# Performance work log

Hardware: AMD Instinct MI355X
Metric: run time of the kernel (lower is better)

The kernel has to match this reference:

```python
import jax, jax.numpy as jnp
import numpy as np

B, S, E, H, V = 64, 400, 512, 512, 32000


def setup_inputs() -> dict:
    key = jax.random.key(0)
    ks = jax.random.split(key, 16)
    sc = lambda fan: 1.0 / np.sqrt(fan)
    u = lambda k, shape, fan: jax.random.uniform(k, shape, jnp.float32, -sc(fan), sc(fan))
    mask = jax.random.randint(ks[3], (B, S), 0, 2).astype(bool)
    mask = mask.at[:, 0].set(True)  # ensure at least one valid position per row
    return {
        "decoder_input": jax.random.normal(ks[0], (B, E), jnp.float32),
        "previous_hidden_state": jax.random.normal(ks[1], (B, H), jnp.float32),
        "encoder_output": jax.random.normal(ks[2], (B, S, 2 * H), jnp.float32),
        "mask": mask,
        # GRUCell params (torch layout: weight_ih [3H,E], weight_hh [3H,H])
        "w_ih": u(ks[4], (3 * H, E), H),
        "w_hh": u(ks[5], (3 * H, H), H),
        "b_ih": u(ks[6], (3 * H,), H),
        "b_hh": u(ks[7], (3 * H,), H),
        # Attention params
        "Wh_w": u(ks[8], (H, 2 * H), 2 * H),
        "Wh_b": u(ks[9], (H,), 2 * H),
        "Ws_w": u(ks[10], (H, H), H),
        "Ws_b": u(ks[11], (H,), H),
        "vatt_w": u(ks[12], (1, H), H),  # Linear(H,1,bias=False)
        # Output projections
        "V_w": u(ks[13], (H, 3 * H), 3 * H),
        "V_b": u(ks[13], (H,), 3 * H),
        "Vhat_w": u(ks[14], (V, H), H),
        "Vhat_b": u(ks[15], (V,), H),
    }


def reference(decoder_input, previous_hidden_state, encoder_output, mask,
              w_ih, w_hh, b_ih, b_hh, Wh_w, Wh_b, Ws_w, Ws_b, vatt_w,
              V_w, V_b, Vhat_w, Vhat_b):
    # --- GRUCell step (torch semantics) ---
    gi = decoder_input @ w_ih.T + b_ih                  # [B, 3H]
    gh = previous_hidden_state @ w_hh.T + b_hh          # [B, 3H]
    i_r, i_z, i_n = jnp.split(gi, 3, axis=-1)
    h_r, h_z, h_n = jnp.split(gh, 3, axis=-1)
    r = jax.nn.sigmoid(i_r + h_r)
    z = jax.nn.sigmoid(i_z + h_z)
    n = jnp.tanh(i_n + r * h_n)
    hidden = (1.0 - z) * n + z * previous_hidden_state  # [B, H]

    # --- Additive (Bahdanau) attention ---
    feat = jnp.tanh(encoder_output @ Wh_w.T + Wh_b
                    + (hidden @ Ws_w.T + Ws_b)[:, None, :])   # [B, S, H]
    scores = jnp.einsum('bsh,h->bs', feat, vatt_w[0])          # [B, S]
    scores = jnp.where(mask, scores, -jnp.inf)
    attn_dist = jax.nn.softmax(scores, axis=-1)                # [B, S]

    # --- Context + output projection ---
    context_vector = jnp.einsum('bs,bsd->bd', attn_dist, encoder_output)  # [B, 2H]
    out = jnp.concatenate([hidden, context_vector], axis=-1) @ V_w.T + V_b  # [B, H]
    logits = out @ Vhat_w.T + Vhat_b                                        # [B, V]
    vocab_dist = jax.nn.softmax(logits, axis=-1)
    return (vocab_dist, attn_dist, context_vector, hidden)
```

## Files before the change

### kernel.cpp

```cpp
#include <hip/hip_runtime.h>
#include <hip/hip_bf16.h>
#include <stdint.h>

#define DI __device__ __forceinline__

using f32x2 = __attribute__((ext_vector_type(2))) float;
using f32x4 = __attribute__((ext_vector_type(4))) float;
using s16x8 = __attribute__((ext_vector_type(8))) short;

#define BB 64
#define SS 400
#define HH 512
#define VVOC 32000
#define MTOT (BB*SS)

DI short bf16r(float f){
  __hip_bfloat16 h = __float2bfloat16(f);
  union { __hip_bfloat16 h; short s; } u; u.h = h; return u.s;
}
DI float sigm(float x){ return 1.f/(1.f + __expf(-x)); }
DI float tanhfast(float x){ x = fminf(x, 12.f); float e = __expf(2.f*x); return (e-1.f)/(e+1.f); }

DI void gload16b(const __hip_bfloat16* g, short* l){
  __builtin_amdgcn_global_load_lds(
      (const __attribute__((address_space(1))) __hip_bfloat16*)g,
      (__attribute__((address_space(3))) short*)l, 16, 0, 0);
}

DI float blkmax(float v, float* red, int t){
  #pragma unroll
  for (int o = 32; o; o >>= 1) v = fmaxf(v, __shfl_xor(v, o));
  if ((t & 63) == 0) red[t >> 6] = v;
  __syncthreads();
  v = fmaxf(fmaxf(red[0], red[1]), fmaxf(red[2], red[3]));
  __syncthreads();
  return v;
}
DI float blksum(float v, float* red, int t){
  #pragma unroll
  for (int o = 32; o; o >>= 1) v += __shfl_xor(v, o);
  if ((t & 63) == 0) red[t >> 6] = v;
  __syncthreads();
  v = red[0] + red[1] + red[2] + red[3];
  __syncthreads();
  return v;
}

DI s16x8 cvt8v(f32x4 a, f32x4 b){
  s16x8 o;
  o[0]=bf16r(a[0]); o[1]=bf16r(a[1]); o[2]=bf16r(a[2]); o[3]=bf16r(a[3]);
  o[4]=bf16r(b[0]); o[5]=bf16r(b[1]); o[6]=bf16r(b[2]); o[7]=bf16r(b[3]);
  return o;
}
DI s16x8 cvt8(const float* src){
  return cvt8v(((const f32x4*)src)[0], ((const f32x4*)src)[1]);
}

DI s16x8 fragload16(const short* tile, int rbase, int kk, int l){
  int r = rbase + (l & 15);
  int c = (kk >> 3) + (l >> 4);
  int slot = c ^ (r & 7);
  return *(const s16x8*)(tile + r*64 + slot*8);
}

DI void mfma_small_body(const float* __restrict__ A, const float* __restrict__ W,
                        float* __restrict__ P, int K, int N, int c0, int kseg,
                        short* lsa, short* lsb, int t)
{
  const int kbeg = kseg*64;
  const int l = t & 63, w = t >> 6;
  #pragma unroll
  for (int q = 0; q < 2; ++q) {
    int it = q*256 + t;
    int r = it >> 3, c = it & 7;
    int slot = (c ^ (r & 7)) << 3;
    *(s16x8*)(lsa + r*64 + slot) = cvt8(A + (size_t)r*K + kbeg + c*8);
    *(s16x8*)(lsb + r*64 + slot) = cvt8(W + (size_t)(c0 + r)*K + kbeg + c*8);
  }
  __syncthreads();
  f32x4 acc[4];
  #pragma unroll
  for (int m = 0; m < 4; ++m) { f32x4 z = {0.f,0.f,0.f,0.f}; acc[m] = z; }
  #pragma unroll
  for (int kk = 0; kk < 64; kk += 32) {
    s16x8 bf = fragload16(lsb, w*16, kk, l);
    #pragma unroll
    for (int m = 0; m < 4; ++m) {
      s16x8 af = fragload16(lsa, m*16, kk, l);
      acc[m] = __builtin_amdgcn_mfma_f32_16x16x32_bf16(af, bf, acc[m], 0, 0, 0);
    }
  }
  const int kq = l >> 4, lc = l & 15;
  const int col = c0 + w*16 + lc;
  size_t pbase = (size_t)kseg * 64 * N;
  #pragma unroll
  for (int m = 0; m < 4; ++m)
    #pragma unroll
    for (int j = 0; j < 4; ++j)
      P[pbase + (size_t)(m*16 + kq*4 + j)*N + col] = acc[m][j];
}

__global__ __launch_bounds__(256) void k_pre(
    const float* __restrict__ wh, short* __restrict__ wh16,
    const unsigned int* __restrict__ mask, int mwords, int* __restrict__ flags,
    const float* __restrict__ x, const float* __restrict__ hprev,
    const float* __restrict__ w_ih, const float* __restrict__ w_hh,
    float* __restrict__ GI, float* __restrict__ GH)
{
  __shared__ __align__(16) short ls[2][64*64];
  int b = blockIdx.x, t = threadIdx.x;
  if (b < 256) {
    int i = b*256 + t;
    ((s16x8*)wh16)[i] = cvt8(wh + (size_t)i*8);
  } else if (b < 264) {
    __shared__ int f;
    if (t == 0) f = 0;
    __syncthreads();
    int loc = 0;
    for (int i = (b-256)*256 + t; i < mwords; i += 8*256) loc |= (mask[i] > 1u) ? 1 : 0;
    if (loc) atomicOr(&f, 1);
    __syncthreads();
    if (t == 0) flags[b-256] = f;
  } else {
    int gb = b - 264;
    int colI = gb % 24;
    int kseg = (gb / 24) % 8;
    int z    = gb / 192;
    mfma_small_body(z ? hprev : x, z ? w_hh : w_ih, z ? GH : GI,
                    512, 1536, colI*64, kseg, ls[0], ls[1], t);
  }
}

__global__ void gru_gate(const float* __restrict__ GI, const float* __restrict__ GH,
                         const float* __restrict__ b_ih, const float* __restrict__ b_hh,
                         const float* __restrict__ hprev, float* __restrict__ hid,
                         float* __restrict__ concat)
{
  int i = blockIdx.x*256 + threadIdx.x;
  int b = i >> 9, h = i & 511;
  float ir=0, iz=0, inn=0, hr=0, hz=0, hn=0;
  #pragma unroll
  for (int s = 0; s < 8; ++s) {
    const float* gi = GI + (size_t)s*(64*1536) + b*1536;
    const float* gh = GH + (size_t)s*(64*1536) + b*1536;
    ir += gi[h];      iz += gi[512+h];  inn += gi[1024+h];
    hr += gh[h];      hz += gh[512+h];  hn  += gh[1024+h];
  }
  ir += b_ih[h]; iz += b_ih[512+h]; inn += b_ih[1024+h];
  hr += b_hh[h]; hz += b_hh[512+h]; hn  += b_hh[1024+h];
  float r = sigm(ir + hr), z = sigm(iz + hz);
  float n = tanhfast(inn + r*hn);
  float hv = (1.f - z)*n + z*hprev[i];
  hid[i] = hv;
  concat[b*1536 + h] = hv;
}

__global__ __launch_bounds__(256) void mfma_small(
    const float* __restrict__ A, const float* __restrict__ W,
    float* __restrict__ P, int K, int N)
{
  __shared__ __align__(16) short ls[2][64*64];
  mfma_small_body(A, W, P, K, N, blockIdx.x*64, blockIdx.y, ls[0], ls[1], threadIdx.x);
}

__global__ void combineN(const float* __restrict__ P, const float* __restrict__ b1,
                         const float* __restrict__ b2, float* __restrict__ dstv,
                         int N, int total, int nseg)
{
  int i = blockIdx.x*256 + threadIdx.x;
  if (i >= total) return;
  float a = 0.f;
  for (int s = 0; s < nseg; ++s) a += P[(size_t)s*total + i];
  int c = i % N;
  if (b1) a += b1[c];
  if (b2) a += b2[c];
  dstv[i] = a;
}

__global__ __launch_bounds__(512, 2) void score_gemm_bf16(
    const float* __restrict__ A, const __hip_bfloat16* __restrict__ Bw,
    const float* __restrict__ qv, const float* __restrict__ vb, float* __restrict__ dst)
{
  __shared__ __align__(16) short lsa[2][128*64];
  __shared__ __align__(16) short lsb[2][512*64];
  const int t = threadIdx.x;
  const int l = t & 63;
  const int w = t >> 6;
  const int wm = w >> 2;
  const int wn = w & 3;
  const int phys = blockIdx.x;
  const int logical = (phys & 7)*25 + (phys >> 3);
  const int mrow = logical * 128;

  f32x4 par[2][2];
  #define A_LOAD(k0)                                                              \
    _Pragma("unroll")                                                             \
    for (int q = 0; q < 2; ++q) {                                                 \
      int ci = q*512 + t; int r = ci >> 3, c = ci & 7;                            \
      const f32x4* ap = (const f32x4*)(A + (size_t)(mrow + r)*1024 + (k0) + c*8); \
      par[q][0] = ap[0]; par[q][1] = ap[1];                                       \
    }
  #define A_WRITE(buf)                                                            \
    _Pragma("unroll")                                                             \
    for (int q = 0; q < 2; ++q) {                                                 \
      int ci = q*512 + t; int r = ci >> 3, c = ci & 7;                            \
      *(s16x8*)(lsa[buf] + r*64 + ((c ^ (r & 7)) << 3)) = cvt8v(par[q][0], par[q][1]); \
    }
  #define B_STAGE(buf, k0)                                                        \
    _Pragma("unroll")                                                             \
    for (int i = 0; i < 8; ++i) {                                                 \
      int ci = i*512 + t; int r = ci >> 3, slot = ci & 7;                         \
      int c = slot ^ (r & 7);                                                     \
      gload16b(Bw + (size_t)r*1024 + (k0) + c*8, lsb[buf] + ci*8);                \
    }

  f32x4 acc[4][8];
  #pragma unroll
  for (int m = 0; m < 4; ++m)
    #pragma unroll
    for (int n = 0; n < 8; ++n) { f32x4 z = {0.f,0.f,0.f,0.f}; acc[m][n] = z; }

  A_LOAD(0)
  A_WRITE(0)
  B_STAGE(0, 0)
  __syncthreads();

  int cur = 0;
  for (int k = 0; k < 16; ++k) {
    if (k < 15) {
      A_LOAD((k+1)*64)
      B_STAGE(cur ^ 1, (k+1)*64)
    }
    __builtin_amdgcn_s_setprio(1);
    #pragma unroll
    for (int kk = 0; kk < 64; kk += 32) {
      s16x8 bf[8];
      #pragma unroll
      for (int n = 0; n < 8; ++n) bf[n] = fragload16(lsb[cur], wn*128 + n*16, kk, l);
      #pragma unroll
      for (int m = 0; m < 4; ++m) {
        s16x8 af = fragload16(lsa[cur], wm*64 + m*16, kk, l);
        #pragma unroll
        for (int n = 0; n < 8; ++n)
          acc[m][n] = __builtin_amdgcn_mfma_f32_16x16x32_bf16(af, bf[n], acc[m][n], 0, 0, 0);
      }
    }
    __builtin_amdgcn_s_setprio(0);
    if (k < 15) A_WRITE(cur ^ 1)
    __syncthreads();
    cur ^= 1;
  }
  #undef A_LOAD
  #undef A_WRITE
  #undef B_STAGE

  const int kq = l >> 4, lc = l & 15;
  float vv[8];
  #pragma unroll
  for (int n = 0; n < 8; ++n) vv[n] = vb[wn*128 + n*16 + lc];
  float* red = (float*)lsa[0];
  #pragma unroll
  for (int m = 0; m < 4; ++m) {
    #pragma unroll
    for (int j = 0; j < 4; ++j) {
      int rl = wm*64 + m*16 + kq*4 + j;
      int r = mrow + rl;
      int b = r / SS;
      const float* qb = qv + b*HH + wn*128 + lc;
      float ps = 0.f;
      #pragma unroll
      for (int n = 0; n < 8; ++n) ps += vv[n]*tanhfast(acc[m][n][j] + qb[n*16]);
      #pragma unroll
      for (int o = 1; o < 16; o <<= 1) ps += __shfl_xor(ps, o);
      if (lc == 0) red[rl*4 + wn] = ps;
    }
  }
  __syncthreads();
  if (t < 128) {
    float s = red[t*4] + red[t*4+1] + red[t*4+2] + red[t*4+3];
    dst[mrow + t] = s;
  }
}

__global__ __launch_bounds__(256) void vocab_gemm(
    const float* __restrict__ OUTm, const float* __restrict__ Vhat,
    const float* __restrict__ Vb, float* __restrict__ logits,
    float* __restrict__ MAXP, float* __restrict__ SUMP)
{
  __shared__ __align__(16) short lsa[64*64];
  __shared__ __align__(16) short lsb[64*64];
  __shared__ float red[64][8];
  const int t = threadIdx.x, l = t & 63, w = t >> 6;
  const int vrow0 = blockIdx.x * 64;

  f32x4 acc[4];
  #pragma unroll
  for (int m = 0; m < 4; ++m) { f32x4 z = {0.f,0.f,0.f,0.f}; acc[m] = z; }

  f32x4 pa0[2][2], pb0[2][2], pa1[2][2], pb1[2][2];

  #define VLOAD(pa, pb, k0)                                                     \
    _Pragma("unroll")                                                           \
    for (int q = 0; q < 2; ++q) {                                               \
      int it = q*256 + t; int r = it >> 3, c = it & 7;                          \
      const f32x4* ap = (const f32x4*)(OUTm + (size_t)r*512 + (k0) + c*8);      \
      pa[q][0] = ap[0]; pa[q][1] = ap[1];                                       \
      const f32x4* bp = (const f32x4*)(Vhat + (size_t)(vrow0 + r)*512 + (k0) + c*8); \
      pb[q][0] = bp[0]; pb[q][1] = bp[1];                                       \
    }
  #define VSTEP(pa, pb)                                                         \
    _Pragma("unroll")                                                           \
    for (int q = 0; q < 2; ++q) {                                               \
      int it = q*256 + t; int r = it >> 3, c = it & 7;                          \
      int slot = (c ^ (r & 7)) << 3;                                            \
      *(s16x8*)(lsa + r*64 + slot) = cvt8v(pa[q][0], pa[q][1]);                 \
      *(s16x8*)(lsb + r*64 + slot) = cvt8v(pb[q][0], pb[q][1]);                 \
    }                                                                           \
    __syncthreads();                                                            \
    _Pragma("unroll")                                                           \
    for (int kk = 0; kk < 64; kk += 32) {                                       \
      s16x8 bf = fragload16(lsb, w*16, kk, l);                                  \
      _Pragma("unroll")                                                         \
      for (int m = 0; m < 4; ++m) {                                             \
        s16x8 af = fragload16(lsa, m*16, kk, l);                                \
        acc[m] = __builtin_amdgcn_mfma_f32_16x16x32_bf16(af, bf, acc[m], 0,0,0);\
      }                                                                         \
    }                                                                           \
    __syncthreads();

  VLOAD(pa0, pb0, 0)
  #pragma unroll
  for (int s2 = 0; s2 < 4; ++s2) {
    int k0 = s2*128;
    if (k0 + 64 < 512) { VLOAD(pa1, pb1, k0 + 64) }
    VSTEP(pa0, pb0)
    if (k0 + 128 < 512) { VLOAD(pa0, pb0, k0 + 128) }
    VSTEP(pa1, pb1)
  }
  #undef VLOAD
  #undef VSTEP

  const int kq = l >> 4, lc = l & 15;
  const int voc = vrow0 + w*16 + lc;
  const float bias = Vb[voc];
  #pragma unroll
  for (int m = 0; m < 4; ++m)
    #pragma unroll
    for (int j = 0; j < 4; ++j) {
      acc[m][j] += bias;
      logits[(size_t)(m*16 + kq*4 + j)*VVOC + voc] = acc[m][j];
    }
  #pragma unroll
  for (int m = 0; m < 4; ++m)
    #pragma unroll
    for (int j = 0; j < 4; ++j) {
      float v = acc[m][j];
      #pragma unroll
      for (int o = 1; o < 16; o <<= 1) v = fmaxf(v, __shfl_xor(v, o));
      if (lc == 0) red[m*16 + kq*4 + j][w] = v;
    }
  __syncthreads();
  float gmax[4][4];
  #pragma unroll
  for (int m = 0; m < 4; ++m)
    #pragma unroll
    for (int j = 0; j < 4; ++j) {
      int row = m*16 + kq*4 + j;
      gmax[m][j] = fmaxf(fmaxf(red[row][0], red[row][1]), fmaxf(red[row][2], red[row][3]));
    }
  __syncthreads();
  #pragma unroll
  for (int m = 0; m < 4; ++m)
    #pragma unroll
    for (int j = 0; j < 4; ++j) {
      float s = __expf(acc[m][j] - gmax[m][j]);
      #pragma unroll
      for (int o = 1; o < 16; o <<= 1) s += __shfl_xor(s, o);
      if (lc == 0) red[m*16 + kq*4 + j][4 + w] = s;
    }
  __syncthreads();
  if (t < 64) {
    float M = fmaxf(fmaxf(red[t][0], red[t][1]), fmaxf(red[t][2], red[t][3]));
    float S = red[t][4] + red[t][5] + red[t][6] + red[t][7];
    MAXP[blockIdx.x*64 + t] = M;
    SUMP[blockIdx.x*64 + t] = S;
  }
}

__global__ __launch_bounds__(256) void vnorm(
    const float* __restrict__ MAXP, const float* __restrict__ SUMP,
    float* __restrict__ logits)
{
  __shared__ float red[4];
  int b = blockIdx.x, q = blockIdx.y, t = threadIdx.x;
  float m = -INFINITY;
  for (int i = t; i < 500; i += 256) m = fmaxf(m, MAXP[i*64 + b]);
  m = blkmax(m, red, t);
  float z = 0.f;
  for (int i = t; i < 500; i += 256) z += SUMP[i*64 + b] * __expf(MAXP[i*64 + b] - m);
  z = blksum(z, red, t);
  float inv = 1.f / z;
  f32x4* p = (f32x4*)(logits + (size_t)b*VVOC + q*8000);
  for (int i = t; i < 2000; i += 256) {
    f32x4 v = p[i];
    #pragma unroll
    for (int c = 0; c < 4; ++c) v[c] = __expf(v[c] - m) * inv;
    p[i] = v;
  }
}

__global__ void softmax_s(const float* __restrict__ score, const void* __restrict__ mask,
                          const int* __restrict__ flags, float* __restrict__ attn)
{
  __shared__ float red[4];
  int b = blockIdx.x, t = threadIdx.x;
  bool isbyte = (flags[0]|flags[1]|flags[2]|flags[3]|flags[4]|flags[5]|flags[6]|flags[7]) != 0;
  float sc0, sc1 = -INFINITY;
  {
    bool mv = isbyte ? (((const unsigned char*)mask)[b*SS + t] != 0)
                     : (((const int*)mask)[b*SS + t] != 0);
    sc0 = mv ? score[b*SS + t] : -INFINITY;
  }
  int s1 = t + 256;
  if (s1 < SS) {
    bool mv = isbyte ? (((const unsigned char*)mask)[b*SS + s1] != 0)
                     : (((const int*)mask)[b*SS + s1] != 0);
    sc1 = mv ? score[b*SS + s1] : -INFINITY;
  }
  float mx = blkmax(fmaxf(sc0, sc1), red, t);
  float e0 = __expf(sc0 - mx), e1 = __expf(sc1 - mx);
  float sum = blksum(e0 + e1, red, t);
  float inv = 1.f / sum;
  attn[b*SS + t] = e0 * inv;
  if (s1 < SS) attn[b*SS + s1] = e1 * inv;
}

__global__ void ctx_part(const float* __restrict__ attn, const float* __restrict__ enc,
                         float* __restrict__ CTXP)
{
  int b = blockIdx.x, dh = blockIdx.y, sq = blockIdx.z;
  int d0 = dh*512 + threadIdx.x*2;
  const float* a = attn + b*SS + sq*50;
  const float* e = enc + (size_t)(b*SS + sq*50)*1024 + d0;
  float lo = 0.f, hi = 0.f;
  #pragma unroll 5
  for (int s = 0; s < 50; ++s) {
    f32x2 u = *(const f32x2*)(e + (size_t)s*1024);
    float av = a[s];
    lo += av * u[0];
    hi += av * u[1];
  }
  float* dst = CTXP + (size_t)sq*65536 + b*1024 + d0;
  dst[0] = lo; dst[1] = hi;
}

__global__ void ctx_combine(const float* __restrict__ CTXP, float* __restrict__ ctx,
                            float* __restrict__ concat)
{
  int b = blockIdx.x;
  for (int d = threadIdx.x; d < 1024; d += 256) {
    float s = 0.f;
    #pragma unroll
    for (int q = 0; q < 8; ++q) s += CTXP[q*65536 + b*1024 + d];
    ctx[b*1024 + d] = s;
    concat[b*1536 + 512 + d] = s;
  }
}

extern "C" void kernel_launch(void* const* d_in, const int* in_sizes, int n_in,
                              void* d_out, int out_size, void* d_ws, size_t ws_size,
                              hipStream_t stream) {
  (void)in_sizes; (void)n_in; (void)out_size; (void)ws_size;
  const float* x      = (const float*)d_in[0];
  const float* hprev  = (const float*)d_in[1];
  const float* enc    = (const float*)d_in[2];
  const void*  mask   = d_in[3];
  const float* w_ih   = (const float*)d_in[4];
  const float* w_hh   = (const float*)d_in[5];
  const float* b_ih   = (const float*)d_in[6];
  const float* b_hh   = (const float*)d_in[7];
  const float* Wh_w   = (const float*)d_in[8];
  const float* Wh_b   = (const float*)d_in[9];
  const float* Ws_w   = (const float*)d_in[10];
  const float* Ws_b   = (const float*)d_in[11];
  const float* vatt   = (const float*)d_in[12];
  const float* V_w    = (const float*)d_in[13];
  const float* V_b    = (const float*)d_in[14];
  const float* Vhat_w = (const float*)d_in[15];
  const float* Vhat_b = (const float*)d_in[16];

  float* out   = (float*)d_out;
  float* vocab = out;
  float* attn  = out + 2048000;
  float* ctx   = out + 2073600;
  float* hid   = out + 2139136;

  float* WS     = (float*)d_ws;
  int*   FLAGS  = (int*)d_ws;
  float* GI     = WS + 16;
  float* GH     = GI + 786432;
  float* QP     = GH + 786432;
  float* Q      = QP + 262144;
  float* OUT    = Q + 32768;
  float* SCORE  = OUT + 32768;
  float* MAXP   = SCORE + 25600;
  float* SUMP   = MAXP + 32000;
  float* CTXP   = SUMP + 32000;
  float* OUTP   = CTXP + 524288;
  float* CONCAT = OUTP + 786432;
  float* ENDF   = CONCAT + 98304;
  size_t f32_bytes = ((size_t)((char*)ENDF - (char*)d_ws) + 15) & ~(size_t)15;
  short* WH16  = (short*)((char*)d_ws + f32_bytes);

  k_pre<<<dim3(648), 256, 0, stream>>>(Wh_w, WH16, (const unsigned int*)mask, 6400, FLAGS,
                                       x, hprev, w_ih, w_hh, GI, GH);
  gru_gate<<<dim3(128), 256, 0, stream>>>(GI, GH, b_ih, b_hh, hprev, hid, CONCAT);
  mfma_small<<<dim3(8, 8), 256, 0, stream>>>(hid, Ws_w, QP, 512, 512);
  combineN<<<dim3(128), 256, 0, stream>>>(QP, Ws_b, Wh_b, Q, 512, 32768, 8);
  score_gemm_bf16<<<dim3(200), 512, 0, stream>>>(
      enc, (const __hip_bfloat16*)WH16, Q, vatt, SCORE);
  softmax_s<<<dim3(64), 256, 0, stream>>>(SCORE, mask, FLAGS, attn);
  ctx_part<<<dim3(64, 2, 8), 256, 0, stream>>>(attn, enc, CTXP);
  ctx_combine<<<dim3(64), 256, 0, stream>>>(CTXP, ctx, CONCAT);
  mfma_small<<<dim3(8, 24), 256, 0, stream>>>(CONCAT, V_w, OUTP, 1536, 512);
  combineN<<<dim3(128), 256, 0, stream>>>(OUTP, V_b, nullptr, OUT, 512, 32768, 24);
  vocab_gemm<<<dim3(500), 256, 0, stream>>>(OUT, Vhat_w, Vhat_b, vocab, MAXP, SUMP);
  vnorm<<<dim3(64, 4), 256, 0, stream>>>(MAXP, SUMP, vocab);
}
```

Before: 135.6 us.

## Triple-buffer score GEMM with direct-to-LDS fp32 A loads and vmcnt waits

Restructures the score GEMM main loop from a two-stage K=64 pipeline into a three-stage K=32 pipeline. The fp32 encoder tile now goes straight from global memory to LDS through global_load_lds and is converted to bf16 when fragments are read, so the A data no longer passes through registers before being written back. Synchronisation switches from __syncthreads to explicit s_waitcnt vmcnt counts plus s_barrier, which lets two stages of loads stay in flight. The cost is more LDS (fp32 A tiles in three buffers), a conversion on every fragment read, twice as many barriers, and hand-tuned vmcnt counts that must match the number of issued loads.

After: 138.8 us. +2.3%, slower.

```diff
diff --git a/kernel.cpp b/kernel.cpp
--- a/kernel.cpp
+++ b/kernel.cpp
@@ -25,6 +25,11 @@
   __builtin_amdgcn_global_load_lds(
       (const __attribute__((address_space(1))) __hip_bfloat16*)g,
       (__attribute__((address_space(3))) short*)l, 16, 0, 0);
+}
+DI void gload16f(const float* g, float* l){
+  __builtin_amdgcn_global_load_lds(
+      (const __attribute__((address_space(1))) float*)g,
+      (__attribute__((address_space(3))) float*)l, 16, 0, 0);
 }
 
 DI float blkmax(float v, float* red, int t){
@@ -181,8 +186,8 @@
     const float* __restrict__ A, const __hip_bfloat16* __restrict__ Bw,
     const float* __restrict__ qv, const float* __restrict__ vb, float* __restrict__ dst)
 {
-  __shared__ __align__(16) short lsa[2][128*64];
-  __shared__ __align__(16) short lsb[2][512*64];
+  __shared__ __align__(16) float lsa[3*4096];
+  __shared__ __align__(16) short lsb[3*16384];
   const int t = threadIdx.x;
   const int l = t & 63;
   const int w = t >> 6;
@@ -192,26 +197,18 @@
   const int logical = (phys & 7)*25 + (phys >> 3);
   const int mrow = logical * 128;
 
-  f32x4 par[2][2];
-  #define A_LOAD(k0)                                                              \
-    _Pragma("unroll")                                                             \
-    for (int q = 0; q < 2; ++q) {                                                 \
-      int ci = q*512 + t; int r = ci >> 3, c = ci & 7;                            \
-      const f32x4* ap = (const f32x4*)(A + (size_t)(mrow + r)*1024 + (k0) + c*8); \
-      par[q][0] = ap[0]; par[q][1] = ap[1];                                       \
-    }
-  #define A_WRITE(buf)                                                            \
-    _Pragma("unroll")                                                             \
-    for (int q = 0; q < 2; ++q) {                                                 \
-      int ci = q*512 + t; int r = ci >> 3, c = ci & 7;                            \
-      *(s16x8*)(lsa[buf] + r*64 + ((c ^ (r & 7)) << 3)) = cvt8v(par[q][0], par[q][1]); \
-    }
-  #define B_STAGE(buf, k0)                                                        \
-    _Pragma("unroll")                                                             \
-    for (int i = 0; i < 8; ++i) {                                                 \
-      int ci = i*512 + t; int r = ci >> 3, slot = ci & 7;                         \
-      int c = slot ^ (r & 7);                                                     \
-      gload16b(Bw + (size_t)r*1024 + (k0) + c*8, lsb[buf] + ci*8);                \
+  #define STAGE(aoff, boff, k0)                                                     \
+    _Pragma("unroll")                                                               \
+    for (int q = 0; q < 2; ++q) {                                                   \
+      int ci = q*512 + t; int r = ci >> 3, slot = ci & 7;                           \
+      int c = slot ^ (r & 7);                                                       \
+      gload16f(A + (size_t)(mrow + r)*1024 + (k0) + c*4, lsa + (aoff) + ci*4);      \
+    }                                                                               \
+    _Pragma("unroll")                                                               \
+    for (int q = 0; q < 4; ++q) {                                                   \
+      int ci = q*512 + t; int r = ci >> 2, slot = ci & 3;                           \
+      int c = slot ^ (r & 3);                                                       \
+      gload16b(Bw + (size_t)r*1024 + (k0) + c*8, lsb + (boff) + ci*8);              \
     }
 
   f32x4 acc[4][8];
@@ -220,45 +217,57 @@
     #pragma unroll
     for (int n = 0; n < 8; ++n) { f32x4 z = {0.f,0.f,0.f,0.f}; acc[m][n] = z; }
 
-  A_LOAD(0)
-  A_WRITE(0)
-  B_STAGE(0, 0)
-  __syncthreads();
+  STAGE(0, 0, 0)
+  STAGE(4096, 16384, 32)
+  asm volatile("s_waitcnt vmcnt(6)" ::: "memory");
+  __builtin_amdgcn_s_barrier();
+  __builtin_amdgcn_sched_barrier(0);
 
   int cur = 0;
-  for (int k = 0; k < 16; ++k) {
-    if (k < 15) {
-      A_LOAD((k+1)*64)
-      B_STAGE(cur ^ 1, (k+1)*64)
-    }
+  for (int k = 0; k < 32; ++k) {
+    if (k + 2 < 32) {
+      int st = (cur >= 1) ? cur - 1 : 2;
+      STAGE(st*4096, st*16384, (k+2)*32)
+    }
+    __builtin_amdgcn_sched_barrier(0);
+    const float* aB = lsa + cur*4096;
+    const short* bB = lsb + cur*16384;
     __builtin_amdgcn_s_setprio(1);
-    #pragma unroll
-    for (int kk = 0; kk < 64; kk += 32) {
+    {
       s16x8 bf[8];
       #pragma unroll
-      for (int n = 0; n < 8; ++n) bf[n] = fragload16(lsb[cur], wn*128 + n*16, kk, l);
+      for (int n = 0; n < 8; ++n) {
+        int r = wn*128 + n*16 + (l & 15);
+        int slot = (l >> 4) ^ (r & 3);
+        bf[n] = *(const s16x8*)(bB + r*32 + slot*8);
+      }
       #pragma unroll
       for (int m = 0; m < 4; ++m) {
-        s16x8 af = fragload16(lsa[cur], wm*64 + m*16, kk, l);
+        int r = wm*64 + m*16 + (l & 15);
+        int kq = l >> 4;
+        const float* base = aB + r*32;
+        f32x4 lo = *(const f32x4*)(base + (((2*kq    ) ^ (r & 7)) << 2));
+        f32x4 hi = *(const f32x4*)(base + (((2*kq + 1) ^ (r & 7)) << 2));
+        s16x8 af = cvt8v(lo, hi);
         #pragma unroll
         for (int n = 0; n < 8; ++n)
           acc[m][n] = __builtin_amdgcn_mfma_f32_16x16x32_bf16(af, bf[n], acc[m][n], 0, 0, 0);
       }
     }
     __builtin_amdgcn_s_setprio(0);
-    if (k < 15) A_WRITE(cur ^ 1)
-    __syncthreads();
-    cur ^= 1;
-  }
-  #undef A_LOAD
-  #undef A_WRITE
-  #undef B_STAGE
+    if (k < 30) asm volatile("s_waitcnt vmcnt(6)" ::: "memory");
+    else        asm volatile("s_waitcnt vmcnt(0)" ::: "memory");
+    __builtin_amdgcn_s_barrier();
+    __builtin_amdgcn_sched_barrier(0);
+    cur = (cur == 2) ? 0 : cur + 1;
+  }
+  #undef STAGE
 
   const int kq = l >> 4, lc = l & 15;
   float vv[8];
   #pragma unroll
   for (int n = 0; n < 8; ++n) vv[n] = vb[wn*128 + n*16 + lc];
-  float* red = (float*)lsa[0];
+  float* red = (float*)lsa;
   #pragma unroll
   for (int m = 0; m < 4; ++m) {
     #pragma unroll
```

## Interleave score GEMM loads with MFMA phases using explicit barriers and waitcnts

Applied to the files above, without the earlier changes.

Restructures the score GEMM main loop into four MFMA phases per K-tile. Each phase is bracketed by raw s_barrier, setprio and sched_barrier, and the global-to-LDS B loads and A loads for the next tile are spread across those phases with explicit vmcnt waits. A loads now read 64 contiguous bytes per thread, four float4s, instead of two strided chunks. The aim is to overlap memory traffic with MFMA and to cut register pressure by holding fewer fragments at once. The cost is more barriers per iteration and fragile hand-placed waitcnt counts.

New measurement: 150.6 us. +11.1%, slower.

```diff
diff --git a/kernel.cpp b/kernel.cpp
--- a/kernel.cpp
+++ b/kernel.cpp
@@ -188,31 +188,41 @@
   const int w = t >> 6;
   const int wm = w >> 2;
   const int wn = w & 3;
-  const int phys = blockIdx.x;
-  const int logical = (phys & 7)*25 + (phys >> 3);
+  const int logical = ((int)blockIdx.x & 7)*25 + ((int)blockIdx.x >> 3);
   const int mrow = logical * 128;
 
-  f32x4 par[2][2];
-  #define A_LOAD(k0)                                                              \
+  const int ar = t >> 2;
+  const int ac2 = (t & 3)*2;
+  const float* aptr = A + (size_t)(mrow + ar)*1024 + (t & 3)*16;
+  const int as0 = ((ac2    ) ^ (ar & 7)) << 3;
+  const int as1 = ((ac2 + 1) ^ (ar & 7)) << 3;
+
+  f32x4 pa[4];
+  #define A_LOAD(k0) { const f32x4* p = (const f32x4*)(aptr + (k0));              \
+                       pa[0]=p[0]; pa[1]=p[1]; pa[2]=p[2]; pa[3]=p[3]; }
+  #define A_WRITE(buf) { *(s16x8*)(lsa[buf] + ar*64 + as0) = cvt8v(pa[0], pa[1]); \
+                         *(s16x8*)(lsa[buf] + ar*64 + as1) = cvt8v(pa[2], pa[3]); }
+  #define B_GLOAD(buf, k0, q0, nq)                                                \
     _Pragma("unroll")                                                             \
-    for (int q = 0; q < 2; ++q) {                                                 \
-      int ci = q*512 + t; int r = ci >> 3, c = ci & 7;                            \
-      const f32x4* ap = (const f32x4*)(A + (size_t)(mrow + r)*1024 + (k0) + c*8); \
-      par[q][0] = ap[0]; par[q][1] = ap[1];                                       \
-    }
-  #define A_WRITE(buf)                                                            \
-    _Pragma("unroll")                                                             \
-    for (int q = 0; q < 2; ++q) {                                                 \
-      int ci = q*512 + t; int r = ci >> 3, c = ci & 7;                            \
-      *(s16x8*)(lsa[buf] + r*64 + ((c ^ (r & 7)) << 3)) = cvt8v(par[q][0], par[q][1]); \
-    }
-  #define B_STAGE(buf, k0)                                                        \
-    _Pragma("unroll")                                                             \
-    for (int i = 0; i < 8; ++i) {                                                 \
-      int ci = i*512 + t; int r = ci >> 3, slot = ci & 7;                         \
+    for (int q = (q0); q < (q0)+(nq); ++q) {                                      \
+      int ci = q*512 + t; int r = ci >> 3, slot = ci & 7;                         \
       int c = slot ^ (r & 7);                                                     \
       gload16b(Bw + (size_t)r*1024 + (k0) + c*8, lsb[buf] + ci*8);                \
     }
+  #define MFMA16(NB)                                                              \
+    _Pragma("unroll")                                                             \
+    for (int m2 = 0; m2 < 4; ++m2) {                                              \
+      _Pragma("unroll")                                                           \
+      for (int j = 0; j < 4; ++j)                                                 \
+        acc[m2][(NB)+j] = __builtin_amdgcn_mfma_f32_16x16x32_bf16(                \
+                              af[m2], bf[j], acc[m2][(NB)+j], 0, 0, 0);           \
+    }
+  #define SYNC_PRE  __builtin_amdgcn_s_barrier();                                 \
+    asm volatile("s_waitcnt lgkmcnt(0)" ::: "memory");                            \
+    __builtin_amdgcn_sched_barrier(0);                                            \
+    __builtin_amdgcn_s_setprio(1);
+  #define SYNC_POST __builtin_amdgcn_s_setprio(0);                                \
+    __builtin_amdgcn_s_barrier();
 
   f32x4 acc[4][8];
   #pragma unroll
@@ -221,38 +231,64 @@
     for (int n = 0; n < 8; ++n) { f32x4 z = {0.f,0.f,0.f,0.f}; acc[m][n] = z; }
 
   A_LOAD(0)
+  B_GLOAD(0, 0, 0, 8)
+  asm volatile("s_waitcnt vmcnt(8)" ::: "memory");
   A_WRITE(0)
-  B_STAGE(0, 0)
-  __syncthreads();
+  asm volatile("s_waitcnt vmcnt(0) lgkmcnt(0)" ::: "memory");
+  __builtin_amdgcn_s_barrier();
 
   int cur = 0;
   for (int k = 0; k < 16; ++k) {
+    const short* aB = lsa[cur];
+    const short* bB = lsb[cur];
+    const int nxt = cur ^ 1;
+    s16x8 af[4], bf[4];
+
+    if (k < 15) { A_LOAD((k+1)*64) B_GLOAD(nxt, (k+1)*64, 0, 2) }
+    #pragma unroll
+    for (int m2 = 0; m2 < 4; ++m2) af[m2] = fragload16(aB, wm*64 + m2*16, 0, l);
+    #pragma unroll
+    for (int j = 0; j < 4; ++j)    bf[j]  = fragload16(bB, wn*128 + j*16, 0, l);
+    SYNC_PRE
+    MFMA16(0)
+    SYNC_POST
+
+    if (k < 15) { B_GLOAD(nxt, (k+1)*64, 2, 2) }
+    #pragma unroll
+    for (int j = 0; j < 4; ++j)    bf[j]  = fragload16(bB, wn*128 + (4+j)*16, 0, l);
+    SYNC_PRE
+    MFMA16(4)
+    SYNC_POST
+
     if (k < 15) {
-      A_LOAD((k+1)*64)
-      B_STAGE(cur ^ 1, (k+1)*64)
-    }
-    __builtin_amdgcn_s_setprio(1);
-    #pragma unroll
-    for (int kk = 0; kk < 64; kk += 32) {
-      s16x8 bf[8];
-      #pragma unroll
-      for (int n = 0; n < 8; ++n) bf[n] = fragload16(lsb[cur], wn*128 + n*16, kk, l);
-      #pragma unroll
-      for (int m = 0; m < 4; ++m) {
-        s16x8 af = fragload16(lsa[cur], wm*64 + m*16, kk, l);
-        #pragma unroll
-        for (int n = 0; n < 8; ++n)
-          acc[m][n] = __builtin_amdgcn_mfma_f32_16x16x32_bf16(af, bf[n], acc[m][n], 0, 0, 0);
-      }
-    }
+      B_GLOAD(nxt, (k+1)*64, 4, 4)
+      asm volatile("s_waitcnt vmcnt(8)" ::: "memory");
+      A_WRITE(nxt)
+    }
+    #pragma unroll
+    for (int m2 = 0; m2 < 4; ++m2) af[m2] = fragload16(aB, wm*64 + m2*16, 32, l);
+    #pragma unroll
+    for (int j = 0; j < 4; ++j)    bf[j]  = fragload16(bB, wn*128 + j*16, 32, l);
+    SYNC_PRE
+    MFMA16(0)
+    SYNC_POST
+
+    #pragma unroll
+    for (int j = 0; j < 4; ++j)    bf[j]  = fragload16(bB, wn*128 + (4+j)*16, 32, l);
+    SYNC_PRE
+    MFMA16(4)
     __builtin_amdgcn_s_setprio(0);
-    if (k < 15) A_WRITE(cur ^ 1)
-    __syncthreads();
+    if (k < 15) asm volatile("s_waitcnt vmcnt(0)" ::: "memory");
+    asm volatile("s_waitcnt lgkmcnt(0)" ::: "memory");
+    __builtin_amdgcn_s_barrier();
     cur ^= 1;
   }
   #undef A_LOAD
   #undef A_WRITE
-  #undef B_STAGE
+  #undef B_GLOAD
+  #undef MFMA16
+  #undef SYNC_PRE
+  #undef SYNC_POST
 
   const int kq = l >> 4, lc = l & 15;
   float vv[8];
```
